# Performance work log

Measured on AMD Instinct MI355X. Metric: run time of the kernel, lower is better.

The kernel has to match this reference:

```python
import jax, jax.numpy as jnp
import numpy as np

B, C, WS, HK = 32, 384, 7, 8           # batch, channels, window size, windows per side
NB, NH, HID = 2, 12, 1536              # num blocks, heads, mlp hidden (4*C)
H = W = HK * WS                        # 56
EPS = 1e-6


def _rel_pos_index(ws: int) -> np.ndarray:
    # Replicates the torch loop: tmp[dy-y+off, dx-x+off] with python negative-index wrap.
    rd = 2 * ws - 1
    a = np.arange(ws)
    qy, qx, ky, kx = np.meshgrid(a, a, a, a, indexing='ij')
    idx = ((ky - qy + ws // 2) % rd) * rd + ((kx - qx + ws // 2) % rd)
    return idx.reshape(ws * ws, ws * ws)


def setup_inputs() -> dict:
    key = jax.random.key(0)
    ks = jax.random.split(key, 12)
    s = 0.02
    inp = {
        'cls_tokens': jax.random.normal(ks[0], (B, C, HK, HK), jnp.float32),
        'patch_tokens': jax.random.normal(ks[1], (B, C, H, W), jnp.float32),
        'qkv_w': s * jax.random.normal(ks[2], (NB, 3 * C, C), jnp.float32),
        'qkv_b': jnp.zeros((NB, 3 * C), jnp.float32),
        'proj_w': s * jax.random.normal(ks[3], (NB, C, C), jnp.float32),
        'proj_b': jnp.zeros((NB, C), jnp.float32),
        'rel_pos': s * jax.random.normal(ks[4], (NB, NH, (2 * WS - 1) ** 2), jnp.float32),
        'ln0_w': jnp.ones((NB, C), jnp.float32), 'ln0_b': jnp.zeros((NB, C), jnp.float32),
        'ln1_w': jnp.ones((NB, C), jnp.float32), 'ln1_b': jnp.zeros((NB, C), jnp.float32),
        'ln2_w': jnp.ones((NB, C), jnp.float32), 'ln2_b': jnp.zeros((NB, C), jnp.float32),
        'mlp_w1': s * jax.random.normal(ks[5], (NB, HID, C), jnp.float32),
        'mlp_b1': jnp.zeros((NB, HID), jnp.float32),
        'mlp_w2': s * jax.random.normal(ks[6], (NB, C, HID), jnp.float32),
        'mlp_b2': jnp.zeros((NB, C), jnp.float32),
    }
    return inp


def _ln(x, w, b):
    m = x.mean(-1, keepdims=True)
    v = ((x - m) ** 2).mean(-1, keepdims=True)
    return (x - m) * jax.lax.rsqrt(v + EPS) * w + b


def _forward(cls_tokens, patch_tokens, qkv_w, qkv_b, proj_w, proj_b, rel_pos,
             ln0_w, ln0_b, ln1_w, ln1_b, ln2_w, ln2_b, mlp_w1, mlp_b1, mlp_w2, mlp_b2):
    hd = C // NH
    scale = hd ** -0.5
    NP = WS * WS  # patch tokens per window

    idx = _rel_pos_index(WS)                                 # [49,49] static
    rp = rel_pos[:, :, idx.reshape(-1)].reshape(NB, NH, NP, NP)
    rp = jnp.pad(rp, ((0, 0), (0, 0), (1, 0), (1, 0)))       # zero bias on cls row/col

    # Projection is Identity (in==out channels, pool=False).
    # convert_to_flatten_layout (no padding needed: H % (HK*WS) == 0)
    p = patch_tokens.reshape(B, C, HK, WS, HK, WS).transpose(0, 2, 4, 3, 5, 1)
    p = p.reshape(B * HK * HK, NP, C)                        # [Bw, 49, C]
    c = cls_tokens.transpose(0, 2, 3, 1).reshape(B * HK * HK, 1, C)
    out = jnp.concatenate([c, p], axis=1)                    # [Bw, 50, C]

    def attn(x, i, patch_attn):
        bx, n, _ = x.shape
        qkv = (x @ qkv_w[i].T + qkv_b[i]).reshape(bx, n, 3, NH, hd).transpose(2, 0, 3, 1, 4)
        q, k, v = qkv[0], qkv[1], qkv[2]
        a = jnp.einsum('bhnd,bhmd->bhnm', q, k) * scale
        if patch_attn:
            a = a + rp[i]
        a = jax.nn.softmax(a, axis=-1)
        o = jnp.einsum('bhnm,bhmd->bhnd', a, v).transpose(0, 2, 1, 3).reshape(bx, n, C)
        return o @ proj_w[i].T + proj_b[i]

    for i in range(NB):
        # cls-token (region) attention across windows of one image
        ct = out[:, 0:1, :].reshape(B, HK * HK, C)
        ct = ct + attn(_ln(ct, ln0_w[i], ln0_b[i]), i, False)
        out = jnp.concatenate([ct.reshape(-1, 1, C), out[:, 1:, :]], axis=1)
        # windowed attention with rel-pos bias
        out = out + attn(_ln(out, ln1_w[i], ln1_b[i]), i, True)
        # MLP (expand is Identity since in==out channels)
        h = _ln(out, ln2_w[i], ln2_b[i])
        h = jax.nn.gelu(h @ mlp_w1[i].T + mlp_b1[i], approximate=False)
        out = out + (h @ mlp_w2[i].T + mlp_b2[i])

    # convert_to_spatial_layout
    cls_out = out[:, 0].reshape(B, HK, HK, C).transpose(0, 3, 1, 2)
    patch_out = out[:, 1:].reshape(B, HK, HK, WS, WS, C).transpose(0, 5, 1, 3, 2, 4).reshape(B, C, H, W)
    return cls_out, patch_out


def reference(cls_tokens, patch_tokens, qkv_w, qkv_b, proj_w, proj_b, rel_pos,
              ln0_w, ln0_b, ln1_w, ln1_b, ln2_w, ln2_b, mlp_w1, mlp_b1, mlp_w2, mlp_b2):
    return _forward(cls_tokens, patch_tokens, qkv_w, qkv_b, proj_w, proj_b, rel_pos,
                    ln0_w, ln0_b, ln1_w, ln1_b, ln2_w, ln2_b, mlp_w1, mlp_b1, mlp_w2, mlp_b2)
```

## Files before the change

### kernel.cpp

```cpp
#include <hip/hip_runtime.h>
#include <hip/hip_bf16.h>
#include <cstdint>
#include <cstddef>

#define BB    32
#define CC    384
#define NHH   12
#define HDD   32
#define WSS   7
#define HKK   8
#define NBB   2
#define HIDD  1536
#define NTT   50
#define NWW   2048
#define LDOUT 19200
#define N3    1152

typedef __attribute__((ext_vector_type(8))) short short8v;
typedef __attribute__((ext_vector_type(4))) float f32x4;

#if defined(__has_builtin)
#if __has_builtin(__builtin_amdgcn_global_load_lds)
#define HAS_GLDS 1
#endif
#endif
#ifndef HAS_GLDS
#define HAS_GLDS 0
#endif

static __device__ __forceinline__ float gelu_f(float x) {
    return 0.5f * x * (1.0f + erff(x * 0.70710678118654752440f));
}

static __device__ __forceinline__ short bf16s(float x) {
    __hip_bfloat16 b = __float2bfloat16(x);
    return *(short*)&b;
}

#if HAS_GLDS
static __device__ __forceinline__ void glds16(const short* g, short* l) {
    __builtin_amdgcn_global_load_lds(
        (const __attribute__((address_space(1))) unsigned int*)g,
        (__attribute__((address_space(3))) unsigned int*)l,
        16, 0, 0);
}
#endif

static __device__ __forceinline__ void swz_decode(int L, int nx, int ny, int& bx, int& by) {
    if (ny & 7) {
        bx = L % nx; by = L / nx;
    } else {
        int r = L & 7, pos = L >> 3;
        bx = pos % nx;
        by = (pos / nx) * 8 + r;
    }
}

__global__ void pack_cls_kernel(const float* __restrict__ cls, float* __restrict__ out) {
    __shared__ float lds[64][65];
    int bid = blockIdx.x;
    int b = bid / 6, cc = bid % 6, c0 = cc * 64;
    int tid = threadIdx.x;
    for (int idx = tid; idx < 64 * 64; idx += 256) {
        int k = idx & 63, cl = idx >> 6;
        lds[cl][k] = cls[((size_t)b * CC + c0 + cl) * 64 + k];
    }
    __syncthreads();
    for (int idx = tid; idx < 64 * 64; idx += 256) {
        int cl = idx & 63, k = idx >> 6;
        out[(size_t)(b * 64 + k) * LDOUT + c0 + cl] = lds[cl][k];
    }
}

__global__ void pack_patch_kernel(const float* __restrict__ patch, float* __restrict__ out) {
    __shared__ float lds[64][57];
    int bid = blockIdx.x;
    int b = bid / 336, rem = bid % 336;
    int y = rem / 6, cc = rem % 6, c0 = cc * 64;
    int tid = threadIdx.x;
    for (int idx = tid; idx < 64 * 56; idx += 256) {
        int cl = idx / 56, x = idx % 56;
        lds[cl][x] = patch[(((size_t)b * CC + c0 + cl) * 56 + y) * 56 + x];
    }
    __syncthreads();
    int wsy = y % 7, hky = y / 7;
    for (int idx = tid; idx < 64 * 56; idx += 256) {
        int cl = idx & 63, x = idx >> 6;
        int tok = 1 + wsy * 7 + (x % 7);
        int win = b * 64 + hky * 8 + (x / 7);
        out[((size_t)win * NTT + tok) * CC + c0 + cl] = lds[cl][x];
    }
}

__global__ void unpack_cls_kernel(const float* __restrict__ out, float* __restrict__ cls_out) {
    __shared__ float lds[64][65];
    int bid = blockIdx.x;
    int b = bid / 6, cc = bid % 6, c0 = cc * 64;
    int tid = threadIdx.x;
    for (int idx = tid; idx < 64 * 64; idx += 256) {
        int cl = idx & 63, k = idx >> 6;
        lds[cl][k] = out[(size_t)(b * 64 + k) * LDOUT + c0 + cl];
    }
    __syncthreads();
    for (int idx = tid; idx < 64 * 64; idx += 256) {
        int k = idx & 63, cl = idx >> 6;
        cls_out[((size_t)b * CC + c0 + cl) * 64 + k] = lds[cl][k];
    }
}

__global__ void unpack_patch_kernel(const float* __restrict__ out, float* __restrict__ patch_out) {
    __shared__ float lds[64][57];
    int bid = blockIdx.x;
    int b = bid / 336, rem = bid % 336;
    int y = rem / 6, cc = rem % 6, c0 = cc * 64;
    int tid = threadIdx.x;
    int wsy = y % 7, hky = y / 7;
    for (int idx = tid; idx < 64 * 56; idx += 256) {
        int cl = idx & 63, x = idx >> 6;
        int tok = 1 + wsy * 7 + (x % 7);
        int win = b * 64 + hky * 8 + (x / 7);
        lds[cl][x] = out[((size_t)win * NTT + tok) * CC + c0 + cl];
    }
    __syncthreads();
    for (int idx = tid; idx < 64 * 56; idx += 256) {
        int cl = idx / 56, x = idx % 56;
        patch_out[((size_t)b * CC + c0 + cl) * 3136 + y * 56 + x] = lds[cl][x];
    }
}

__global__ void f2bf_kernel(const float* __restrict__ in, __hip_bfloat16* __restrict__ out, int n) {
    int i = (blockIdx.x * 256 + threadIdx.x) * 4;
    if (i + 3 < n) {
        float4 v = *(const float4*)(in + i);
        out[i + 0] = __float2bfloat16(v.x);
        out[i + 1] = __float2bfloat16(v.y);
        out[i + 2] = __float2bfloat16(v.z);
        out[i + 3] = __float2bfloat16(v.w);
    } else {
        for (; i < n; ++i) out[i] = __float2bfloat16(in[i]);
    }
}

__global__ void bias_precompute_kernel(const float* __restrict__ rp, float* __restrict__ biasT) {
    int h = blockIdx.x;
    for (int idx = threadIdx.x; idx < 4096; idx += 256) {
        int qt = idx >> 6, kt = idx & 63;
        float v = 0.f;
        if (qt >= 1 && qt < NTT && kt >= 1 && kt < NTT) {
            int qp = qt - 1, kp = kt - 1;
            int qy = qp / 7, qx = qp - qy * 7;
            int ky = kp / 7, kx = kp - ky * 7;
            int ridx = ((ky - qy + 16) % 13) * 13 + ((kx - qx + 16) % 13);
            v = rp[h * 169 + ridx];
        }
        biasT[h * 4096 + qt * 64 + (kt & 15) * 4 + (kt >> 4)] = v;
    }
}

__global__ void ln_kernel(const float* __restrict__ x, int ldx,
                          const float* __restrict__ w, const float* __restrict__ b,
                          __hip_bfloat16* __restrict__ y, int ldy, int M) {
    int wave = threadIdx.x >> 6, lane = threadIdx.x & 63;
    int row = blockIdx.x * 4 + wave;
    if (row >= M) return;
    const float2* xr = (const float2*)(x + (size_t)row * ldx);
    float2 vals[3];
    float s = 0.f;
#pragma unroll
    for (int j = 0; j < 3; ++j) { vals[j] = xr[lane + j * 64]; s += vals[j].x + vals[j].y; }
#pragma unroll
    for (int off = 32; off > 0; off >>= 1) s += __shfl_xor(s, off);
    float mean = s * (1.0f / 384.0f);
    float vs = 0.f;
#pragma unroll
    for (int j = 0; j < 3; ++j) {
        float dx = vals[j].x - mean, dy = vals[j].y - mean;
        vs += dx * dx + dy * dy;
    }
#pragma unroll
    for (int off = 32; off > 0; off >>= 1) vs += __shfl_xor(vs, off);
    float inv = rsqrtf(vs * (1.0f / 384.0f) + 1e-6f);
    const float2* w2 = (const float2*)w;
    const float2* b2 = (const float2*)b;
    ushort* yr = (ushort*)(y + (size_t)row * ldy);
#pragma unroll
    for (int j = 0; j < 3; ++j) {
        int c = lane + j * 64;
        float2 wv = w2[c], bv = b2[c];
        ushort2 o;
        o.x = (ushort)bf16s((vals[j].x - mean) * inv * wv.x + bv.x);
        o.y = (ushort)bf16s((vals[j].y - mean) * inv * wv.y + bv.y);
        *(ushort2*)(yr + c * 2) = o;
    }
}

template <int BIAS, int GELU, int ACC, int OUTBF>
__global__ __launch_bounds__(512, 4) void gemm_bf16_kernel(
    const __hip_bfloat16* __restrict__ A, int lda,
    const __hip_bfloat16* __restrict__ W,
    const float* __restrict__ bias,
    float* __restrict__ Y, int ldy,
    __hip_bfloat16* __restrict__ Yb, int ldyb,
    int M, int N, int K, int nx) {
    __shared__ __align__(16) union SMemU {
        struct { short As[3][256 * 32]; short Bs[3][128 * 32]; } st;
        short obf[256][132];
        float off[128][132];
    } sm;
    int tid = threadIdx.x;
    int lane = tid & 63;
    int wid = tid >> 6;
    int wr = wid >> 1, wc = wid & 1;
    int bx, by;
    swz_decode(blockIdx.x, nx, M >> 8, bx, by);
    int row0 = by * 256, col0 = bx * 128;

    const short* Ag = (const short*)A + (size_t)(row0 + wid * 32 + (lane >> 2)) * lda + (lane & 3) * 8;
    const short* Wg = (const short*)W + (size_t)(col0 + wid * 16 + (lane >> 2)) * K + (lane & 3) * 8;
    size_t astep16 = (size_t)16 * lda;
    int ldsA = wid * 32 * 32;
    int ldsB = wid * 16 * 32;

#if HAS_GLDS
#define STAGE(buf, k0)                                                \
    do {                                                              \
        glds16(Ag + (k0), &sm.st.As[buf][ldsA]);                      \
        glds16(Ag + astep16 + (k0), &sm.st.As[buf][ldsA + 16 * 32]);  \
        glds16(Wg + (k0), &sm.st.Bs[buf][ldsB]);                      \
    } while (0)
#else
#define STAGE(buf, k0)                                                               \
    do {                                                                             \
        *(short8v*)(&sm.st.As[buf][ldsA] + lane * 8) = *(const short8v*)(Ag + (k0)); \
        *(short8v*)(&sm.st.As[buf][ldsA + 16 * 32] + lane * 8) = *(const short8v*)(Ag + astep16 + (k0)); \
        *(short8v*)(&sm.st.Bs[buf][ldsB] + lane * 8) = *(const short8v*)(Wg + (k0)); \
    } while (0)
#endif

    f32x4 acc[4][4] = {};
    int frow_a = wr * 64 + (lane & 15);
    int frow_b = wc * 64 + (lane & 15);
    int fk = (lane >> 4) * 8;

    int nt = K >> 5;
#if HAS_GLDS
    STAGE(0, 0);
    if (nt > 1) STAGE(1, 32);
    int sc = 0;
    for (int t = 0; t < nt; ++t) {
        int sn = sc + 2; if (sn >= 3) sn -= 3;
        if (t + 2 < nt) {
            STAGE(sn, (t + 2) << 5);
            asm volatile("s_waitcnt vmcnt(6)" ::: "memory");
        } else if (t + 1 < nt) {
            asm volatile("s_waitcnt vmcnt(3)" ::: "memory");
        } else {
            asm volatile("s_waitcnt vmcnt(0)" ::: "memory");
        }
        __builtin_amdgcn_s_barrier();
        __builtin_amdgcn_sched_barrier(0);
        short8v a[4], b[4];
#pragma unroll
        for (int m = 0; m < 4; ++m) a[m] = *(const short8v*)&sm.st.As[sc][(frow_a + m * 16) * 32 + fk];
#pragma unroll
        for (int n = 0; n < 4; ++n) b[n] = *(const short8v*)&sm.st.Bs[sc][(frow_b + n * 16) * 32 + fk];
        __builtin_amdgcn_s_setprio(1);
#pragma unroll
        for (int m = 0; m < 4; ++m)
#pragma unroll
            for (int n = 0; n < 4; ++n)
                acc[m][n] = __builtin_amdgcn_mfma_f32_16x16x32_bf16(a[m], b[n], acc[m][n], 0, 0, 0);
        __builtin_amdgcn_s_setprio(0);
        __builtin_amdgcn_sched_barrier(0);
        __builtin_amdgcn_s_barrier();
        ++sc; if (sc >= 3) sc = 0;
    }
#else
    STAGE(0, 0);
    __syncthreads();
    int cur = 0;
    for (int t = 0; t < nt; ++t) {
        if (t + 1 < nt) STAGE(cur ^ 1, (t + 1) << 5);
        short8v a[4], b[4];
#pragma unroll
        for (int m = 0; m < 4; ++m) a[m] = *(const short8v*)&sm.st.As[cur][(frow_a + m * 16) * 32 + fk];
#pragma unroll
        for (int n = 0; n < 4; ++n) b[n] = *(const short8v*)&sm.st.Bs[cur][(frow_b + n * 16) * 32 + fk];
#pragma unroll
        for (int m = 0; m < 4; ++m)
#pragma unroll
            for (int n = 0; n < 4; ++n)
                acc[m][n] = __builtin_amdgcn_mfma_f32_16x16x32_bf16(a[m], b[n], acc[m][n], 0, 0, 0);
        if (t + 1 < nt) { __syncthreads(); cur ^= 1; }
    }
#endif
#undef STAGE

    __syncthreads();
    int lr = (lane >> 4) * 4;
    int lc = lane & 15;
    if (OUTBF) {
#pragma unroll
        for (int n = 0; n < 4; ++n) {
            int c = wc * 64 + n * 16 + lc;
            float bv = BIAS ? bias[col0 + c] : 0.0f;
#pragma unroll
            for (int m = 0; m < 4; ++m) {
#pragma unroll
                for (int j = 0; j < 4; ++j) {
                    float v = acc[m][n][j] + bv;
                    if (GELU) v = gelu_f(v);
                    sm.obf[wr * 64 + m * 16 + lr + j][c] = bf16s(v);
                }
            }
        }
        __syncthreads();
        short* yb = (short*)Yb + (size_t)row0 * ldyb + col0;
#pragma unroll
        for (int it = 0; it < 8; ++it) {
            int r = (tid >> 4) + it * 32;
            int c8 = (tid & 15) * 8;
            *(short8v*)(yb + (size_t)r * ldyb + c8) = *(const short8v*)&sm.obf[r][c8];
        }
    } else {
#pragma unroll
        for (int half = 0; half < 2; ++half) {
            if (half) __syncthreads();
            if ((wr >> 1) == half) {
#pragma unroll
                for (int n = 0; n < 4; ++n) {
                    int c = wc * 64 + n * 16 + lc;
                    float bv = BIAS ? bias[col0 + c] : 0.0f;
#pragma unroll
                    for (int m = 0; m < 4; ++m)
#pragma unroll
                        for (int j = 0; j < 4; ++j) {
                            float v = acc[m][n][j] + bv;
                            if (GELU) v = gelu_f(v);
                            sm.off[(wr & 1) * 64 + m * 16 + lr + j][c] = v;
                        }
                }
            }
            __syncthreads();
            float* yp0 = Y + (size_t)(row0 + half * 128) * ldy + col0;
#pragma unroll
            for (int it = 0; it < 8; ++it) {
                int r = (tid >> 5) + it * 16;
                int c4 = (tid & 31) * 4;
                float4 v = *(const float4*)&sm.off[r][c4];
                float* yp = yp0 + (size_t)r * ldy + c4;
                if (ACC) {
                    float4 o = *(const float4*)yp;
                    v.x += o.x; v.y += o.y; v.z += o.z; v.w += o.w;
                }
                *(float4*)yp = v;
            }
        }
    }
}

__global__ __launch_bounds__(256) void attn_mfma_kernel(
    const __hip_bfloat16* __restrict__ qkv,
    const float* __restrict__ biasT,
    __hip_bfloat16* __restrict__ o,
    int T, float scale, int nwin) {
    __shared__ __align__(16) short Vt[4][32][72];
    __shared__ __align__(16) short Pl[4][64][40];
    const int tid = threadIdx.x, lane = tid & 63, wv = tid >> 6;
    int p, hg;
    {
        int L = blockIdx.x;
        if (nwin & 7) { hg = L % 3; p = L / 3; }
        else { int r = L & 7, pos = L >> 3; hg = pos % 3; p = (pos / 3) * 8 + r; }
    }
    const int h = hg * 4 + wv;
    const short* q_base = (const short*)qkv + (size_t)p * T * N3;

    const int fr = lane & 15;
    const int fk = (lane >> 4) * 8;
    const int lg = lane >> 4;
    const int lc = lane & 15;

    short8v aq[4], bk[4];
#pragma unroll
    for (int m = 0; m < 4; ++m) {
        const short* qp = q_base + (size_t)(m * 16 + fr) * N3 + h * 32 + fk;
        aq[m] = *(const short8v*)qp;
        bk[m] = *(const short8v*)(qp + 384);
    }

    for (int ch = lane; ch < T * 4; ch += 64) {
        int t = ch >> 2, cq = ch & 3;
        short8v v8 = *(const short8v*)(q_base + (size_t)t * N3 + 768 + h * 32 + cq * 8);
#pragma unroll
        for (int e = 0; e < 8; ++e) Vt[wv][cq * 8 + e][t] = v8[e];
    }
    for (int idx = lane; idx < (64 - T) * 32; idx += 64) {
        int t = T + (idx >> 5), d = idx & 31;
        Vt[wv][d][t] = 0;
    }

    f32x4 acc[4][4] = {};
#pragma unroll
    for (int m = 0; m < 4; ++m)
#pragma unroll
        for (int n = 0; n < 4; ++n)
            acc[m][n] = __builtin_amdgcn_mfma_f32_16x16x32_bf16(aq[m], bk[n], acc[m][n], 0, 0, 0);

    const float* bh = biasT ? (biasT + (size_t)h * 4096) : nullptr;
    float p2[4][4], p3[4][4];
#pragma unroll
    for (int m = 0; m < 4; ++m) {
#pragma unroll
        for (int j = 0; j < 4; ++j) {
            int r = m * 16 + lg * 4 + j;
            float v[4];
            if (bh) {
                float4 bv4 = *(const float4*)(bh + r * 64 + lc * 4);
#pragma unroll
                for (int n = 0; n < 4; ++n) v[n] = acc[m][n][j] * scale + ((const float*)&bv4)[n];
            } else {
#pragma unroll
                for (int n = 0; n < 4; ++n) v[n] = acc[m][n][j] * scale;
            }
#pragma unroll
            for (int n = 0; n < 4; ++n)
                if (n * 16 + lc >= T) v[n] = -1e30f;
            float mx = fmaxf(fmaxf(v[0], v[1]), fmaxf(v[2], v[3]));
#pragma unroll
            for (int off = 1; off < 16; off <<= 1) mx = fmaxf(mx, __shfl_xor(mx, off));
            float s = 0.f;
#pragma unroll
            for (int n = 0; n < 4; ++n) { v[n] = __expf(v[n] - mx); s += v[n]; }
#pragma unroll
            for (int off = 1; off < 16; off <<= 1) s += __shfl_xor(s, off);
            float inv = 1.0f / s;
            Pl[wv][r][lc]      = bf16s(v[0] * inv);
            Pl[wv][r][16 + lc] = bf16s(v[1] * inv);
            p2[m][j] = v[2] * inv;
            p3[m][j] = v[3] * inv;
        }
    }

    f32x4 oacc[4][2] = {};
    {
        short8v ap[4], bv[2];
#pragma unroll
        for (int m = 0; m < 4; ++m) ap[m] = *(const short8v*)&Pl[wv][m * 16 + fr][fk];
#pragma unroll
        for (int n = 0; n < 2; ++n) bv[n] = *(const short8v*)&Vt[wv][n * 16 + fr][fk];
#pragma unroll
        for (int m = 0; m < 4; ++m)
#pragma unroll
            for (int n = 0; n < 2; ++n)
                oacc[m][n] = __builtin_amdgcn_mfma_f32_16x16x32_bf16(ap[m], bv[n], oacc[m][n], 0, 0, 0);
    }
#pragma unroll
    for (int m = 0; m < 4; ++m)
#pragma unroll
        for (int j = 0; j < 4; ++j) {
            int r = m * 16 + lg * 4 + j;
            Pl[wv][r][lc]      = bf16s(p2[m][j]);
            Pl[wv][r][16 + lc] = bf16s(p3[m][j]);
        }
    {
        short8v ap[4], bv[2];
#pragma unroll
        for (int m = 0; m < 4; ++m) ap[m] = *(const short8v*)&Pl[wv][m * 16 + fr][fk];
#pragma unroll
        for (int n = 0; n < 2; ++n) bv[n] = *(const short8v*)&Vt[wv][n * 16 + fr][32 + fk];
#pragma unroll
        for (int m = 0; m < 4; ++m)
#pragma unroll
            for (int n = 0; n < 2; ++n)
                oacc[m][n] = __builtin_amdgcn_mfma_f32_16x16x32_bf16(ap[m], bv[n], oacc[m][n], 0, 0, 0);
    }

    short* ob = (short*)o;
#pragma unroll
    for (int m = 0; m < 4; ++m)
#pragma unroll
        for (int j = 0; j < 4; ++j) {
            int r = m * 16 + lg * 4 + j;
            if (r < T) {
#pragma unroll
                for (int n = 0; n < 2; ++n)
                    ob[((size_t)p * T + r) * CC + h * 32 + n * 16 + lc] = bf16s(oacc[m][n][j]);
            }
        }
}

extern "C" void kernel_launch(void* const* d_in, const int* in_sizes, int n_in,
                              void* d_out, int out_size, void* d_ws, size_t ws_size,
                              hipStream_t stream) {
    const float* cls_in   = (const float*)d_in[0];
    const float* patch_in = (const float*)d_in[1];
    const float* qkv_w    = (const float*)d_in[2];
    const float* qkv_b    = (const float*)d_in[3];
    const float* proj_w   = (const float*)d_in[4];
    const float* proj_b   = (const float*)d_in[5];
    const float* rel_pos  = (const float*)d_in[6];
    const float* ln0w = (const float*)d_in[7];
    const float* ln0b = (const float*)d_in[8];
    const float* ln1w = (const float*)d_in[9];
    const float* ln1b = (const float*)d_in[10];
    const float* ln2w = (const float*)d_in[11];
    const float* ln2b = (const float*)d_in[12];
    const float* w1 = (const float*)d_in[13];
    const float* b1 = (const float*)d_in[14];
    const float* w2 = (const float*)d_in[15];
    const float* b2 = (const float*)d_in[16];

    float* OUT = (float*)d_ws;
    size_t avail = ws_size / 4;

    const size_t OUT_F = 39321600;
    const size_t WB_F  = 1769472;
    const size_t BT_F  = 49152;
    __hip_bfloat16* WB = (__hip_bfloat16*)(OUT + OUT_F);
    __hip_bfloat16* qwb = WB;
    __hip_bfloat16* pwb = WB + 884736;
    __hip_bfloat16* w1b = WB + 1179648;
    __hip_bfloat16* w2b = WB + 2359296;
    float* biasTbuf = OUT + OUT_F + WB_F;

    int cw = 1024;
    while (cw > 128 && OUT_F + WB_F + BT_F + (size_t)cw * 48000 > avail) cw >>= 1;
    float* fbase = OUT + OUT_F + WB_F + BT_F;
    __hip_bfloat16* Xb = (__hip_bfloat16*)fbase;
    __hip_bfloat16* Qb = (__hip_bfloat16*)(fbase + (size_t)cw * 9600);
    __hip_bfloat16* Hb = Qb;
    const float scale = 0.17677669529663687f;

    f2bf_kernel<<<dim3((884736 / 4 + 255) / 256), dim3(256), 0, stream>>>(qkv_w, qwb, 884736);
    f2bf_kernel<<<dim3((294912 / 4 + 255) / 256), dim3(256), 0, stream>>>(proj_w, pwb, 294912);
    f2bf_kernel<<<dim3((1179648 / 4 + 255) / 256), dim3(256), 0, stream>>>(w1, w1b, 1179648);
    f2bf_kernel<<<dim3((1179648 / 4 + 255) / 256), dim3(256), 0, stream>>>(w2, w2b, 1179648);

    pack_cls_kernel<<<dim3(BB * 6), dim3(256), 0, stream>>>(cls_in, OUT);
    pack_patch_kernel<<<dim3(BB * 56 * 6), dim3(256), 0, stream>>>(patch_in, OUT);

    for (int i = 0; i < NBB; ++i) {
        const __hip_bfloat16* qw = qwb + (size_t)i * N3 * CC;
        const float* qb = qkv_b + (size_t)i * N3;
        const __hip_bfloat16* pw = pwb + (size_t)i * CC * CC;
        const float* pb = proj_b + (size_t)i * CC;
        const float* rp = rel_pos + (size_t)i * NHH * 169;
        const __hip_bfloat16* w1i = w1b + (size_t)i * HIDD * CC;
        const float* b1i = b1 + (size_t)i * HIDD;
        const __hip_bfloat16* w2i = w2b + (size_t)i * CC * HIDD;
        const float* b2i = b2 + (size_t)i * CC;

        bias_precompute_kernel<<<dim3(NHH), dim3(256), 0, stream>>>(rp, biasTbuf);

        ln_kernel<<<dim3(2048 / 4), dim3(256), 0, stream>>>(OUT, LDOUT, ln0w + i * CC, ln0b + i * CC, Xb, CC, 2048);
        gemm_bf16_kernel<1, 0, 0, 1><<<dim3((N3 / 128) * (2048 / 256)), dim3(512), 0, stream>>>(
            Xb, CC, qw, qb, nullptr, 0, Qb, N3, 2048, N3, CC, N3 / 128);
        attn_mfma_kernel<<<dim3(BB * 3), dim3(256), 0, stream>>>(Qb, nullptr, Xb, 64, scale, BB);
        gemm_bf16_kernel<1, 0, 1, 0><<<dim3((CC / 128) * (2048 / 256)), dim3(512), 0, stream>>>(
            Xb, CC, pw, pb, OUT, LDOUT, nullptr, 0, 2048, CC, CC, CC / 128);

        for (int w0 = 0; w0 < NWW; w0 += cw) {
            float* outc = OUT + (size_t)w0 * LDOUT;
            int Mr = cw * NTT;
            ln_kernel<<<dim3(Mr / 4), dim3(256), 0, stream>>>(outc, CC, ln1w + i * CC, ln1b + i * CC, Xb, CC, Mr);
            gemm_bf16_kernel<1, 0, 0, 1><<<dim3((N3 / 128) * (Mr / 256)), dim3(512), 0, stream>>>(
                Xb, CC, qw, qb, nullptr, 0, Qb, N3, Mr, N3, CC, N3 / 128);
            attn_mfma_kernel<<<dim3(cw * 3), dim3(256), 0, stream>>>(Qb, biasTbuf, Xb, NTT, scale, cw);
            gemm_bf16_kernel<1, 0, 1, 0><<<dim3((CC / 128) * (Mr / 256)), dim3(512), 0, stream>>>(
                Xb, CC, pw, pb, outc, CC, nullptr, 0, Mr, CC, CC, CC / 128);
        }

        for (int w0 = 0; w0 < NWW; w0 += cw) {
            float* outc = OUT + (size_t)w0 * LDOUT;
            int Mr = cw * NTT;
            ln_kernel<<<dim3(Mr / 4), dim3(256), 0, stream>>>(outc, CC, ln2w + i * CC, ln2b + i * CC, Xb, CC, Mr);
            gemm_bf16_kernel<1, 1, 0, 1><<<dim3((HIDD / 128) * (Mr / 256)), dim3(512), 0, stream>>>(
                Xb, CC, w1i, b1i, nullptr, 0, Hb, HIDD, Mr, HIDD, CC, HIDD / 128);
            gemm_bf16_kernel<1, 0, 1, 0><<<dim3((CC / 128) * (Mr / 256)), dim3(512), 0, stream>>>(
                Hb, HIDD, w2i, b2i, outc, CC, nullptr, 0, Mr, CC, HIDD, CC / 128);
        }
    }

    unpack_cls_kernel<<<dim3(BB * 6), dim3(256), 0, stream>>>(OUT, (float*)d_out);
    unpack_patch_kernel<<<dim3(BB * 56 * 6), dim3(256), 0, stream>>>(OUT, (float*)d_out + 786432);
}
```

Before: 2.073 ms.

## Deepen GEMM pipeline to BK=64 halves with XOR-swizzled LDS and interleaved staging

```diff
diff --git a/kernel.cpp b/kernel.cpp
--- a/kernel.cpp
+++ b/kernel.cpp
@@ -195,7 +195,7 @@
 }
 
 template <int BIAS, int GELU, int ACC, int OUTBF>
-__global__ __launch_bounds__(512, 4) void gemm_bf16_kernel(
+__global__ __launch_bounds__(512, 2) void gemm_bf16_kernel(
     const __hip_bfloat16* __restrict__ A, int lda,
     const __hip_bfloat16* __restrict__ W,
     const float* __restrict__ bias,
@@ -203,7 +203,7 @@
     __hip_bfloat16* __restrict__ Yb, int ldyb,
     int M, int N, int K, int nx) {
     __shared__ __align__(16) union SMemU {
-        struct { short As[3][256 * 32]; short Bs[3][128 * 32]; } st;
+        struct { short sA[3][2][256 * 32]; short sB[3][2][128 * 32]; } st;
         short obf[256][132];
         float off[128][132];
     } sm;
@@ -215,86 +215,99 @@
     swz_decode(blockIdx.x, nx, M >> 8, bx, by);
     int row0 = by * 256, col0 = bx * 128;
 
-    const short* Ag = (const short*)A + (size_t)(row0 + wid * 32 + (lane >> 2)) * lda + (lane & 3) * 8;
-    const short* Wg = (const short*)W + (size_t)(col0 + wid * 16 + (lane >> 2)) * K + (lane & 3) * 8;
+    int srow = lane >> 2;
+    int scg = ((lane & 3) ^ (srow & 3)) * 8;
+    const short* Ag = (const short*)A + (size_t)(row0 + wid * 32 + srow) * lda + scg;
+    const short* Wg = (const short*)W + (size_t)(col0 + wid * 16 + srow) * K + scg;
     size_t astep16 = (size_t)16 * lda;
-    int ldsA = wid * 32 * 32;
-    int ldsB = wid * 16 * 32;
-
-#if HAS_GLDS
-#define STAGE(buf, k0)                                                \
-    do {                                                              \
-        glds16(Ag + (k0), &sm.st.As[buf][ldsA]);                      \
-        glds16(Ag + astep16 + (k0), &sm.st.As[buf][ldsA + 16 * 32]);  \
-        glds16(Wg + (k0), &sm.st.Bs[buf][ldsB]);                      \
-    } while (0)
-#else
-#define STAGE(buf, k0)                                                               \
-    do {                                                                             \
-        *(short8v*)(&sm.st.As[buf][ldsA] + lane * 8) = *(const short8v*)(Ag + (k0)); \
-        *(short8v*)(&sm.st.As[buf][ldsA + 16 * 32] + lane * 8) = *(const short8v*)(Ag + astep16 + (k0)); \
-        *(short8v*)(&sm.st.Bs[buf][ldsB] + lane * 8) = *(const short8v*)(Wg + (k0)); \
-    } while (0)
-#endif
 
     f32x4 acc[4][4] = {};
     int frow_a = wr * 64 + (lane & 15);
     int frow_b = wc * 64 + (lane & 15);
-    int fk = (lane >> 4) * 8;
-
-    int nt = K >> 5;
+    int fks = ((lane >> 4) ^ (lane & 3)) * 8;
+
+    int nt = K >> 6;
+
 #if HAS_GLDS
-    STAGE(0, 0);
-    if (nt > 1) STAGE(1, 32);
+#define STAGEH(b, h, k0)                                                    \
+    do {                                                                    \
+        glds16(Ag + (k0) + (h) * 32, &sm.st.sA[b][h][wid * 1024]);          \
+        glds16(Ag + astep16 + (k0) + (h) * 32, &sm.st.sA[b][h][wid * 1024 + 512]); \
+        glds16(Wg + (k0) + (h) * 32, &sm.st.sB[b][h][wid * 512]);           \
+    } while (0)
+
+    STAGEH(0, 0, 0);  STAGEH(0, 1, 0);
+    STAGEH(1, 0, 64); STAGEH(1, 1, 64);
     int sc = 0;
     for (int t = 0; t < nt; ++t) {
         int sn = sc + 2; if (sn >= 3) sn -= 3;
-        if (t + 2 < nt) {
-            STAGE(sn, (t + 2) << 5);
-            asm volatile("s_waitcnt vmcnt(6)" ::: "memory");
-        } else if (t + 1 < nt) {
-            asm volatile("s_waitcnt vmcnt(3)" ::: "memory");
-        } else {
-            asm volatile("s_waitcnt vmcnt(0)" ::: "memory");
-        }
+        int k2 = (t + 2) << 6;
+        if (t + 1 < nt) asm volatile("s_waitcnt vmcnt(9)" ::: "memory");
+        else            asm volatile("s_waitcnt vmcnt(3)" ::: "memory");
         __builtin_amdgcn_s_barrier();
-        __builtin_amdgcn_sched_barrier(0);
-        short8v a[4], b[4];
-#pragma unroll
-        for (int m = 0; m < 4; ++m) a[m] = *(const short8v*)&sm.st.As[sc][(frow_a + m * 16) * 32 + fk];
-#pragma unroll
-        for (int n = 0; n < 4; ++n) b[n] = *(const short8v*)&sm.st.Bs[sc][(frow_b + n * 16) * 32 + fk];
-        __builtin_amdgcn_s_setprio(1);
-#pragma unroll
-        for (int m = 0; m < 4; ++m)
-#pragma unroll
-            for (int n = 0; n < 4; ++n)
-                acc[m][n] = __builtin_amdgcn_mfma_f32_16x16x32_bf16(a[m], b[n], acc[m][n], 0, 0, 0);
-        __builtin_amdgcn_s_setprio(0);
-        __builtin_amdgcn_sched_barrier(0);
+        {
+            short8v a[4], b[4];
+#pragma unroll
+            for (int m = 0; m < 4; ++m) a[m] = *(const short8v*)&sm.st.sA[sc][0][(frow_a + m * 16) * 32 + fks];
+#pragma unroll
+            for (int n = 0; n < 4; ++n) b[n] = *(const short8v*)&sm.st.sB[sc][0][(frow_b + n * 16) * 32 + fks];
+            if (t + 2 < nt) STAGEH(sn, 0, k2);
+            __builtin_amdgcn_s_setprio(1);
+#pragma unroll
+            for (int m = 0; m < 4; ++m)
+#pragma unroll
+                for (int n = 0; n < 4; ++n)
+                    acc[m][n] = __builtin_amdgcn_mfma_f32_16x16x32_bf16(a[m], b[n], acc[m][n], 0, 0, 0);
+            __builtin_amdgcn_s_setprio(0);
+        }
+        if (t + 2 < nt)      asm volatile("s_waitcnt vmcnt(9)" ::: "memory");
+        else if (t + 1 < nt) asm volatile("s_waitcnt vmcnt(6)" ::: "memory");
+        else                 asm volatile("s_waitcnt vmcnt(0)" ::: "memory");
         __builtin_amdgcn_s_barrier();
+        {
+            short8v a[4], b[4];
+#pragma unroll
+            for (int m = 0; m < 4; ++m) a[m] = *(const short8v*)&sm.st.sA[sc][1][(frow_a + m * 16) * 32 + fks];
+#pragma unroll
+            for (int n = 0; n < 4; ++n) b[n] = *(const short8v*)&sm.st.sB[sc][1][(frow_b + n * 16) * 32 + fks];
+            if (t + 2 < nt) STAGEH(sn, 1, k2);
+            __builtin_amdgcn_s_setprio(1);
+#pragma unroll
+            for (int m = 0; m < 4; ++m)
+#pragma unroll
+                for (int n = 0; n < 4; ++n)
+                    acc[m][n] = __builtin_amdgcn_mfma_f32_16x16x32_bf16(a[m], b[n], acc[m][n], 0, 0, 0);
+            __builtin_amdgcn_s_setprio(0);
+        }
         ++sc; if (sc >= 3) sc = 0;
     }
+#undef STAGEH
 #else
-    STAGE(0, 0);
-    __syncthreads();
-    int cur = 0;
     for (int t = 0; t < nt; ++t) {
-        if (t + 1 < nt) STAGE(cur ^ 1, (t + 1) << 5);
-        short8v a[4], b[4];
-#pragma unroll
-        for (int m = 0; m < 4; ++m) a[m] = *(const short8v*)&sm.st.As[cur][(frow_a + m * 16) * 32 + fk];
-#pragma unroll
-        for (int n = 0; n < 4; ++n) b[n] = *(const short8v*)&sm.st.Bs[cur][(frow_b + n * 16) * 32 + fk];
-#pragma unroll
-        for (int m = 0; m < 4; ++m)
-#pragma unroll
-            for (int n = 0; n < 4; ++n)
-                acc[m][n] = __builtin_amdgcn_mfma_f32_16x16x32_bf16(a[m], b[n], acc[m][n], 0, 0, 0);
-        if (t + 1 < nt) { __syncthreads(); cur ^= 1; }
+        int k0 = t << 6;
+#pragma unroll
+        for (int h = 0; h < 2; ++h) {
+            *(short8v*)(&sm.st.sA[0][h][wid * 1024] + lane * 8) = *(const short8v*)(Ag + k0 + h * 32);
+            *(short8v*)(&sm.st.sA[0][h][wid * 1024 + 512] + lane * 8) = *(const short8v*)(Ag + astep16 + k0 + h * 32);
+            *(short8v*)(&sm.st.sB[0][h][wid * 512] + lane * 8) = *(const short8v*)(Wg + k0 + h * 32);
+        }
+        __syncthreads();
+#pragma unroll
+        for (int h = 0; h < 2; ++h) {
+            short8v a[4], b[4];
+#pragma unroll
+            for (int m = 0; m < 4; ++m) a[m] = *(const short8v*)&sm.st.sA[0][h][(frow_a + m * 16) * 32 + fks];
+#pragma unroll
+            for (int n = 0; n < 4; ++n) b[n] = *(const short8v*)&sm.st.sB[0][h][(frow_b + n * 16) * 32 + fks];
+#pragma unroll
+            for (int m = 0; m < 4; ++m)
+#pragma unroll
+                for (int n = 0; n < 4; ++n)
+                    acc[m][n] = __builtin_amdgcn_mfma_f32_16x16x32_bf16(a[m], b[n], acc[m][n], 0, 0, 0);
+        }
+        __syncthreads();
     }
 #endif
-#undef STAGE
 
     __syncthreads();
     int lr = (lane >> 4) * 4;
@@ -524,7 +537,7 @@
     __hip_bfloat16* w2b = WB + 2359296;
     float* biasTbuf = OUT + OUT_F + WB_F;
 
-    int cw = 1024;
+    int cw = 2048;
     while (cw > 128 && OUT_F + WB_F + BT_F + (size_t)cw * 48000 > avail) cw >>= 1;
     float* fbase = OUT + OUT_F + WB_F + BT_F;
     __hip_bfloat16* Xb = (__hip_bfloat16*)fbase;
```

New measurement: 2.339 ms. 12.9% more time.

## Store residual stream in bf16 and use tanh-approximate GELU

Applied to the files above, without the earlier changes.

```diff
diff --git a/kernel.cpp b/kernel.cpp
--- a/kernel.cpp
+++ b/kernel.cpp
@@ -29,12 +29,21 @@
 #endif
 
 static __device__ __forceinline__ float gelu_f(float x) {
-    return 0.5f * x * (1.0f + erff(x * 0.70710678118654752440f));
+    float t = x * (0.7978845608028654f + 0.03567740814f * x * x);
+    float e = __expf(2.0f * t);
+    float th = 1.0f - 2.0f / (e + 1.0f);
+    return 0.5f * x * (1.0f + th);
 }
 
 static __device__ __forceinline__ short bf16s(float x) {
     __hip_bfloat16 b = __float2bfloat16(x);
     return *(short*)&b;
+}
+
+static __device__ __forceinline__ float bf2f(short s) {
+    union { unsigned int u; float f; } cv;
+    cv.u = ((unsigned int)(unsigned short)s) << 16;
+    return cv.f;
 }
 
 #if HAS_GLDS
@@ -56,7 +65,7 @@
     }
 }
 
-__global__ void pack_cls_kernel(const float* __restrict__ cls, float* __restrict__ out) {
+__global__ void pack_cls_kernel(const float* __restrict__ cls, __hip_bfloat16* __restrict__ out) {
     __shared__ float lds[64][65];
     int bid = blockIdx.x;
     int b = bid / 6, cc = bid % 6, c0 = cc * 64;
@@ -66,13 +75,14 @@
         lds[cl][k] = cls[((size_t)b * CC + c0 + cl) * 64 + k];
     }
     __syncthreads();
+    short* ob = (short*)out;
     for (int idx = tid; idx < 64 * 64; idx += 256) {
         int cl = idx & 63, k = idx >> 6;
-        out[(size_t)(b * 64 + k) * LDOUT + c0 + cl] = lds[cl][k];
-    }
-}
-
-__global__ void pack_patch_kernel(const float* __restrict__ patch, float* __restrict__ out) {
+        ob[(size_t)(b * 64 + k) * LDOUT + c0 + cl] = bf16s(lds[cl][k]);
+    }
+}
+
+__global__ void pack_patch_kernel(const float* __restrict__ patch, __hip_bfloat16* __restrict__ out) {
     __shared__ float lds[64][57];
     int bid = blockIdx.x;
     int b = bid / 336, rem = bid % 336;
@@ -84,22 +94,24 @@
     }
     __syncthreads();
     int wsy = y % 7, hky = y / 7;
+    short* ob = (short*)out;
     for (int idx = tid; idx < 64 * 56; idx += 256) {
         int cl = idx & 63, x = idx >> 6;
         int tok = 1 + wsy * 7 + (x % 7);
         int win = b * 64 + hky * 8 + (x / 7);
-        out[((size_t)win * NTT + tok) * CC + c0 + cl] = lds[cl][x];
-    }
-}
-
-__global__ void unpack_cls_kernel(const float* __restrict__ out, float* __restrict__ cls_out) {
+        ob[((size_t)win * NTT + tok) * CC + c0 + cl] = bf16s(lds[cl][x]);
+    }
+}
+
+__global__ void unpack_cls_kernel(const __hip_bfloat16* __restrict__ out, float* __restrict__ cls_out) {
     __shared__ float lds[64][65];
     int bid = blockIdx.x;
     int b = bid / 6, cc = bid % 6, c0 = cc * 64;
     int tid = threadIdx.x;
+    const short* ob = (const short*)out;
     for (int idx = tid; idx < 64 * 64; idx += 256) {
         int cl = idx & 63, k = idx >> 6;
-        lds[cl][k] = out[(size_t)(b * 64 + k) * LDOUT + c0 + cl];
+        lds[cl][k] = bf2f(ob[(size_t)(b * 64 + k) * LDOUT + c0 + cl]);
     }
     __syncthreads();
     for (int idx = tid; idx < 64 * 64; idx += 256) {
@@ -108,18 +120,19 @@
     }
 }
 
-__global__ void unpack_patch_kernel(const float* __restrict__ out, float* __restrict__ patch_out) {
+__global__ void unpack_patch_kernel(const __hip_bfloat16* __restrict__ out, float* __restrict__ patch_out) {
     __shared__ float lds[64][57];
     int bid = blockIdx.x;
     int b = bid / 336, rem = bid % 336;
     int y = rem / 6, cc = rem % 6, c0 = cc * 64;
     int tid = threadIdx.x;
     int wsy = y % 7, hky = y / 7;
+    const short* ob = (const short*)out;
     for (int idx = tid; idx < 64 * 56; idx += 256) {
         int cl = idx & 63, x = idx >> 6;
         int tok = 1 + wsy * 7 + (x % 7);
         int win = b * 64 + hky * 8 + (x / 7);
-        lds[cl][x] = out[((size_t)win * NTT + tok) * CC + c0 + cl];
+        lds[cl][x] = bf2f(ob[((size_t)win * NTT + tok) * CC + c0 + cl]);
     }
     __syncthreads();
     for (int idx = tid; idx < 64 * 56; idx += 256) {
@@ -157,17 +170,22 @@
     }
 }
 
-__global__ void ln_kernel(const float* __restrict__ x, int ldx,
+__global__ void ln_kernel(const __hip_bfloat16* __restrict__ x, int ldx,
                           const float* __restrict__ w, const float* __restrict__ b,
                           __hip_bfloat16* __restrict__ y, int ldy, int M) {
     int wave = threadIdx.x >> 6, lane = threadIdx.x & 63;
     int row = blockIdx.x * 4 + wave;
     if (row >= M) return;
-    const float2* xr = (const float2*)(x + (size_t)row * ldx);
+    const ushort2* xr = (const ushort2*)((const short*)x + (size_t)row * ldx);
     float2 vals[3];
     float s = 0.f;
 #pragma unroll
-    for (int j = 0; j < 3; ++j) { vals[j] = xr[lane + j * 64]; s += vals[j].x + vals[j].y; }
+    for (int j = 0; j < 3; ++j) {
+        ushort2 u = xr[lane + j * 64];
+        vals[j].x = bf2f((short)u.x);
+        vals[j].y = bf2f((short)u.y);
+        s += vals[j].x + vals[j].y;
+    }
 #pragma unroll
     for (int off = 32; off > 0; off >>= 1) s += __shfl_xor(s, off);
     float mean = s * (1.0f / 384.0f);
@@ -182,7 +200,7 @@
     float inv = rsqrtf(vs * (1.0f / 384.0f) + 1e-6f);
     const float2* w2 = (const float2*)w;
     const float2* b2 = (const float2*)b;
-    ushort* yr = (ushort*)(y + (size_t)row * ldy);
+    ushort* yr = (ushort*)y + (size_t)row * ldy;
 #pragma unroll
     for (int j = 0; j < 3; ++j) {
         int c = lane + j * 64;
@@ -194,18 +212,16 @@
     }
 }
 
-template <int BIAS, int GELU, int ACC, int OUTBF>
+template <int BIAS, int GELU, int ACC>
 __global__ __launch_bounds__(512, 4) void gemm_bf16_kernel(
     const __hip_bfloat16* __restrict__ A, int lda,
     const __hip_bfloat16* __restrict__ W,
     const float* __restrict__ bias,
-    float* __restrict__ Y, int ldy,
     __hip_bfloat16* __restrict__ Yb, int ldyb,
     int M, int N, int K, int nx) {
     __shared__ __align__(16) union SMemU {
         struct { short As[3][256 * 32]; short Bs[3][128 * 32]; } st;
         short obf[256][132];
-        float off[128][132];
     } sm;
     int tid = threadIdx.x;
     int lane = tid & 63;
@@ -299,63 +315,34 @@
     __syncthreads();
     int lr = (lane >> 4) * 4;
     int lc = lane & 15;
-    if (OUTBF) {
-#pragma unroll
-        for (int n = 0; n < 4; ++n) {
-            int c = wc * 64 + n * 16 + lc;
-            float bv = BIAS ? bias[col0 + c] : 0.0f;
-#pragma unroll
-            for (int m = 0; m < 4; ++m) {
-#pragma unroll
-                for (int j = 0; j < 4; ++j) {
-                    float v = acc[m][n][j] + bv;
-                    if (GELU) v = gelu_f(v);
-                    sm.obf[wr * 64 + m * 16 + lr + j][c] = bf16s(v);
-                }
+#pragma unroll
+    for (int n = 0; n < 4; ++n) {
+        int c = wc * 64 + n * 16 + lc;
+        float bv = BIAS ? bias[col0 + c] : 0.0f;
+#pragma unroll
+        for (int m = 0; m < 4; ++m) {
+#pragma unroll
+            for (int j = 0; j < 4; ++j) {
+                float v = acc[m][n][j] + bv;
+                if (GELU) v = gelu_f(v);
+                sm.obf[wr * 64 + m * 16 + lr + j][c] = bf16s(v);
             }
         }
-        __syncthreads();
-        short* yb = (short*)Yb + (size_t)row0 * ldyb + col0;
-#pragma unroll
-        for (int it = 0; it < 8; ++it) {
-            int r = (tid >> 4) + it * 32;
-            int c8 = (tid & 15) * 8;
-            *(short8v*)(yb + (size_t)r * ldyb + c8) = *(const short8v*)&sm.obf[r][c8];
-        }
-    } else {
-#pragma unroll
-        for (int half = 0; half < 2; ++half) {
-            if (half) __syncthreads();
-            if ((wr >> 1) == half) {
-#pragma unroll
-                for (int n = 0; n < 4; ++n) {
-                    int c = wc * 64 + n * 16 + lc;
-                    float bv = BIAS ? bias[col0 + c] : 0.0f;
-#pragma unroll
-                    for (int m = 0; m < 4; ++m)
-#pragma unroll
-                        for (int j = 0; j < 4; ++j) {
-                            float v = acc[m][n][j] + bv;
-                            if (GELU) v = gelu_f(v);
-                            sm.off[(wr & 1) * 64 + m * 16 + lr + j][c] = v;
-                        }
-                }
-            }
-            __syncthreads();
-            float* yp0 = Y + (size_t)(row0 + half * 128) * ldy + col0;
-#pragma unroll
-            for (int it = 0; it < 8; ++it) {
-                int r = (tid >> 5) + it * 16;
-                int c4 = (tid & 31) * 4;
-                float4 v = *(const float4*)&sm.off[r][c4];
-                float* yp = yp0 + (size_t)r * ldy + c4;
-                if (ACC) {
-                    float4 o = *(const float4*)yp;
-                    v.x += o.x; v.y += o.y; v.z += o.z; v.w += o.w;
-                }
-                *(float4*)yp = v;
-            }
-        }
+    }
+    __syncthreads();
+    short* yb = (short*)Yb + (size_t)row0 * ldyb + col0;
+#pragma unroll
+    for (int it = 0; it < 8; ++it) {
+        int r = (tid >> 4) + it * 32;
+        int c8 = (tid & 15) * 8;
+        short8v v = *(const short8v*)&sm.obf[r][c8];
+        short* yp = yb + (size_t)r * ldyb + c8;
+        if (ACC) {
+            short8v o = *(const short8v*)yp;
+#pragma unroll
+            for (int e = 0; e < 8; ++e) v[e] = bf16s(bf2f(v[e]) + bf2f(o[e]));
+        }
+        *(short8v*)yp = v;
     }
 }
 
@@ -511,22 +498,23 @@
     const float* w2 = (const float*)d_in[15];
     const float* b2 = (const float*)d_in[16];
 
-    float* OUT = (float*)d_ws;
+    float* WS = (float*)d_ws;
     size_t avail = ws_size / 4;
 
-    const size_t OUT_F = 39321600;
-    const size_t WB_F  = 1769472;
-    const size_t BT_F  = 49152;
-    __hip_bfloat16* WB = (__hip_bfloat16*)(OUT + OUT_F);
+    const size_t OUT_FB = 19660800;
+    const size_t WB_F   = 1769472;
+    const size_t BT_F   = 49152;
+    __hip_bfloat16* OUTB = (__hip_bfloat16*)WS;
+    __hip_bfloat16* WB = (__hip_bfloat16*)(WS + OUT_FB);
     __hip_bfloat16* qwb = WB;
     __hip_bfloat16* pwb = WB + 884736;
     __hip_bfloat16* w1b = WB + 1179648;
     __hip_bfloat16* w2b = WB + 2359296;
-    float* biasTbuf = OUT + OUT_F + WB_F;
+    float* biasTbuf = WS + OUT_FB + WB_F;
 
     int cw = 1024;
-    while (cw > 128 && OUT_F + WB_F + BT_F + (size_t)cw * 48000 > avail) cw >>= 1;
-    float* fbase = OUT + OUT_F + WB_F + BT_F;
+    while (cw > 128 && OUT_FB + WB_F + BT_F + (size_t)cw * 48000 > avail) cw >>= 1;
+    float* fbase = WS + OUT_FB + WB_F + BT_F;
     __hip_bfloat16* Xb = (__hip_bfloat16*)fbase;
     __hip_bfloat16* Qb = (__hip_bfloat16*)(fbase + (size_t)cw * 9600);
     __hip_bfloat16* Hb = Qb;
@@ -537,8 +525,8 @@
     f2bf_kernel<<<dim3((1179648 / 4 + 255) / 256), dim3(256), 0, stream>>>(w1, w1b, 1179648);
     f2bf_kernel<<<dim3((1179648 / 4 + 255) / 256), dim3(256), 0, stream>>>(w2, w2b, 1179648);
 
-    pack_cls_kernel<<<dim3(BB * 6), dim3(256), 0, stream>>>(cls_in, OUT);
-    pack_patch_kernel<<<dim3(BB * 56 * 6), dim3(256), 0, stream>>>(patch_in, OUT);
+    pack_cls_kernel<<<dim3(BB * 6), dim3(256), 0, stream>>>(cls_in, OUTB);
+    pack_patch_kernel<<<dim3(BB * 56 * 6), dim3(256), 0, stream>>>(patch_in, OUTB);
 
     for (int i = 0; i < NBB; ++i) {
         const __hip_bfloat16* qw = qwb + (size_t)i * N3 * CC;
@@ -553,35 +541,35 @@
 
         bias_precompute_kernel<<<dim3(NHH), dim3(256), 0, stream>>>(rp, biasTbuf);
 
-        ln_kernel<<<dim3(2048 / 4), dim3(256), 0, stream>>>(OUT, LDOUT, ln0w + i * CC, ln0b + i * CC, Xb, CC, 2048);
-        gemm_bf16_kernel<1, 0, 0, 1><<<dim3((N3 / 128) * (2048 / 256)), dim3(512), 0, stream>>>(
-            Xb, CC, qw, qb, nullptr, 0, Qb, N3, 2048, N3, CC, N3 / 128);
+        ln_kernel<<<dim3(2048 / 4), dim3(256), 0, stream>>>(OUTB, LDOUT, ln0w + i * CC, ln0b + i * CC, Xb, CC, 2048);
+        gemm_bf16_kernel<1, 0, 0><<<dim3((N3 / 128) * (2048 / 256)), dim3(512), 0, stream>>>(
+            Xb, CC, qw, qb, Qb, N3, 2048, N3, CC, N3 / 128);
         attn_mfma_kernel<<<dim3(BB * 3), dim3(256), 0, stream>>>(Qb, nullptr, Xb, 64, scale, BB);
-        gemm_bf16_kernel<1, 0, 1, 0><<<dim3((CC / 128) * (2048 / 256)), dim3(512), 0, stream>>>(
-            Xb, CC, pw, pb, OUT, LDOUT, nullptr, 0, 2048, CC, CC, CC / 128);
+        gemm_bf16_kernel<1, 0, 1><<<dim3((CC / 128) * (2048 / 256)), dim3(512), 0, stream>>>(
+            Xb, CC, pw, pb, OUTB, LDOUT, 2048, CC, CC, CC / 128);
 
         for (int w0 = 0; w0 < NWW; w0 += cw) {
-            float* outc = OUT + (size_t)w0 * LDOUT;
+            __hip_bfloat16* outc = OUTB + (size_t)w0 * LDOUT;
             int Mr = cw * NTT;
             ln_kernel<<<dim3(Mr / 4), dim3(256), 0, stream>>>(outc, CC, ln1w + i * CC, ln1b + i * CC, Xb, CC, Mr);
-            gemm_bf16_kernel<1, 0, 0, 1><<<dim3((N3 / 128) * (Mr / 256)), dim3(512), 0, stream>>>(
-                Xb, CC, qw, qb, nullptr, 0, Qb, N3, Mr, N3, CC, N3 / 128);
+            gemm_bf16_kernel<1, 0, 0><<<dim3((N3 / 128) * (Mr / 256)), dim3(512), 0, stream>>>(
+                Xb, CC, qw, qb, Qb, N3, Mr, N3, CC, N3 / 128);
             attn_mfma_kernel<<<dim3(cw * 3), dim3(256), 0, stream>>>(Qb, biasTbuf, Xb, NTT, scale, cw);
-            gemm_bf16_kernel<1, 0, 1, 0><<<dim3((CC / 128) * (Mr / 256)), dim3(512), 0, stream>>>(
-                Xb, CC, pw, pb, outc, CC, nullptr, 0, Mr, CC, CC, CC / 128);
+            gemm_bf16_kernel<1, 0, 1><<<dim3((CC / 128) * (Mr / 256)), dim3(512), 0, stream>>>(
+                Xb, CC, pw, pb, outc, CC, Mr, CC, CC, CC / 128);
         }
 
         for (int w0 = 0; w0 < NWW; w0 += cw) {
-            float* outc = OUT + (size_t)w0 * LDOUT;
+            __hip_bfloat16* outc = OUTB + (size_t)w0 * LDOUT;
             int Mr = cw * NTT;
             ln_kernel<<<dim3(Mr / 4), dim3(256), 0, stream>>>(outc, CC, ln2w + i * CC, ln2b + i * CC, Xb, CC, Mr);
-            gemm_bf16_kernel<1, 1, 0, 1><<<dim3((HIDD / 128) * (Mr / 256)), dim3(512), 0, stream>>>(
-                Xb, CC, w1i, b1i, nullptr, 0, Hb, HIDD, Mr, HIDD, CC, HIDD / 128);
-            gemm_bf16_kernel<1, 0, 1, 0><<<dim3((CC / 128) * (Mr / 256)), dim3(512), 0, stream>>>(
-                Hb, HIDD, w2i, b2i, outc, CC, nullptr, 0, Mr, CC, HIDD, CC / 128);
-        }
-    }
-
-    unpack_cls_kernel<<<dim3(BB * 6), dim3(256), 0, stream>>>(OUT, (float*)d_out);
-    unpack_patch_kernel<<<dim3(BB * 56 * 6), dim3(256), 0, stream>>>(OUT, (float*)d_out + 786432);
-}
+            gemm_bf16_kernel<1, 1, 0><<<dim3((HIDD / 128) * (Mr / 256)), dim3(512), 0, stream>>>(
+                Xb, CC, w1i, b1i, Hb, HIDD, Mr, HIDD, CC, HIDD / 128);
+            gemm_bf16_kernel<1, 0, 1><<<dim3((CC / 128) * (Mr / 256)), dim3(512), 0, stream>>>(
+                Hb, HIDD, w2i, b2i, outc, CC, Mr, CC, HIDD, CC / 128);
+        }
+    }
+
+    unpack_cls_kernel<<<dim3(BB * 6), dim3(256), 0, stream>>>(OUTB, (float*)d_out);
+    unpack_patch_kernel<<<dim3(BB * 56 * 6), dim3(256), 0, stream>>>(OUTB, (float*)d_out + 786432);
+}
```

Result: faster. 1.913 ms (-7.7%).
